# Performance work log

Measured on AMD Instinct MI355X. Metric: run time of the kernel, lower is better.

## Reference

```python
import jax, jax.numpy as jnp
from jax import lax
import numpy as np

B, T, C = 2048, 512, 32  # batch, max_seq_len, num_tags


def setup_inputs() -> dict:
    key = jax.random.key(0)
    k1, k2, k3, k4 = jax.random.split(key, 4)
    logits = jax.random.normal(k1, (B, T, C), dtype=jnp.float32)
    sequence_length = jax.random.randint(k2, (B,), 1, T + 1, dtype=jnp.int32)
    labels = jax.random.randint(k3, (B, T), 0, C, dtype=jnp.int32)
    # learned CRF transition matrix (orthogonal init approximated by normal)
    transitions = jax.random.normal(k4, (C, C), dtype=jnp.float32)
    return dict(logits=logits, sequence_length=sequence_length,
                labels=labels, transitions=transitions)


def _viterbi_decode(logits, transitions, seq_len):
    """tfa_text.crf_decode: returns highest-scoring tag sequence [B, T] int32."""
    Bn, Tn, Cn = logits.shape
    identity_bp = jnp.arange(Cn, dtype=jnp.int32)[None, :]  # carries tag through padding

    def fwd(state, xs):  # state: [B, C] viterbi scores
        logit_t, t = xs
        scores = state[:, :, None] + transitions[None]       # [B, C_prev, C_cur]
        cand = logit_t + jnp.max(scores, axis=1)             # [B, C]
        bp = jnp.argmax(scores, axis=1).astype(jnp.int32)    # [B, C] best prev tag
        active = (t < seq_len)[:, None]
        return (jnp.where(active, cand, state),
                jnp.where(active, bp, identity_bp))

    xs = (jnp.swapaxes(logits[:, 1:], 0, 1), jnp.arange(1, Tn))
    final_state, bps = lax.scan(fwd, logits[:, 0], xs)       # bps: [T-1, B, C]
    last_tag = jnp.argmax(final_state, axis=-1).astype(jnp.int32)  # [B]

    def back(tag, bp):  # tag at t+1 -> tag at t
        prev = jnp.take_along_axis(bp, tag[:, None], axis=1)[:, 0]
        return prev, tag

    first_tag, later_tags = lax.scan(back, last_tag, bps, reverse=True)
    tags = jnp.concatenate([first_tag[None], later_tags], axis=0).T  # [B, T]
    valid = jnp.arange(Tn)[None, :] < seq_len[:, None]
    return jnp.where(valid, tags, 0)


def _crf_log_likelihood(logits, labels, transitions, seq_len):
    """tfa_text.crf_log_likelihood: per-example log-likelihood [B]."""
    Bn, Tn, Cn = logits.shape

    # --- log partition via forward algorithm ---
    def fwd(alpha, xs):
        logit_t, t = xs
        new = jax.nn.logsumexp(alpha[:, :, None] + transitions[None], axis=1) + logit_t
        active = (t < seq_len)[:, None]
        return jnp.where(active, new, alpha), None

    xs = (jnp.swapaxes(logits[:, 1:], 0, 1), jnp.arange(1, Tn))
    alpha, _ = lax.scan(fwd, logits[:, 0], xs)
    log_norm = jax.nn.logsumexp(alpha, axis=-1)  # [B]

    # --- score of gold label sequence ---
    pos = jnp.arange(Tn)
    mask = (pos[None, :] < seq_len[:, None]).astype(logits.dtype)          # [B, T]
    unary = jnp.sum(
        jnp.take_along_axis(logits, labels[..., None], axis=2)[..., 0] * mask,
        axis=1)
    pair_mask = (pos[None, :-1] < (seq_len - 1)[:, None]).astype(logits.dtype)
    binary = jnp.sum(transitions[labels[:, :-1], labels[:, 1:]] * pair_mask, axis=1)

    return unary + binary - log_norm


def reference(logits, sequence_length, labels, transitions):
    # training=True path: labels clamped to >= 0 (already non-negative here)
    labels = jnp.maximum(labels, 0)
    decode_tags = _viterbi_decode(logits, transitions, sequence_length)
    log_likelihood = _crf_log_likelihood(logits, labels, transitions, sequence_length)
    loss = jnp.mean(-log_likelihood)  # recorded via add_loss in the original
    return decode_tags, loss
```

## Files before the change

kernel.cpp:

```cpp
#include <hip/hip_runtime.h>
#include <math.h>

#define BB 2048
#define TT 512
#define CC 32

#if __has_builtin(__builtin_amdgcn_exp2f)
#define EXP2F __builtin_amdgcn_exp2f
#else
#define EXP2F exp2f
#endif
#if __has_builtin(__builtin_amdgcn_logf)
#define LOG2F __builtin_amdgcn_logf
#else
#define LOG2F log2f
#endif

#define LOG2E 1.4426950408889634f
#define LN2   0.6931471805599453f

__global__ void zero_loss_kernel(float* __restrict__ out) {
  if (threadIdx.x == 0) out[(size_t)BB * TT] = 0.0f;
}

__global__ void schedule_kernel(const int* __restrict__ seqlen,
                                int* __restrict__ perm,
                                float* __restrict__ out) {
  __shared__ int s[TT];
  __shared__ int off[TT];
  const int tid = threadIdx.x;
  if (tid == 0) out[(size_t)BB * TT] = 0.0f;
  s[tid] = 0;
  __syncthreads();
  for (int b = tid; b < BB; b += TT) atomicAdd(&s[seqlen[b] - 1], 1);
  __syncthreads();
  for (int d = 1; d < TT; d <<= 1) {
    int v = s[tid] + ((tid + d < TT) ? s[tid + d] : 0);
    __syncthreads();
    s[tid] = v;
    __syncthreads();
  }
  off[tid] = (tid + 1 < TT) ? s[tid + 1] : 0;
  __syncthreads();
  for (int b = tid; b < BB; b += TT) {
    int pos = atomicAdd(&off[seqlen[b] - 1], 1);
    perm[pos] = b;
  }
}

#define ROR(dst, src, K)                                                     \
  dst = __int_as_float(__builtin_amdgcn_update_dpp(                          \
      0, __float_as_int(src), 0x120 | (K), 0xF, 0xF, false));

__global__ __launch_bounds__(128, 4) void crf_kernel(
    const float* __restrict__ logits,
    const int*   __restrict__ seqlen,
    const int*   __restrict__ labels,
    const float* __restrict__ trans,
    float*       __restrict__ out,
    const int*   __restrict__ perm)
{
  __shared__ __align__(16) unsigned char bp_s[(TT - 1) * CC];
  __shared__ __align__(16) float avs[CC];
  __shared__ unsigned char tag_s[TT];

  const int lane = threadIdx.x & 63;
  const int wv   = threadIdx.x >> 6;
  const int k    = blockIdx.x;

  const int bs0 = perm ? perm[k] : k;
  const int bs1 = perm ? perm[BB - 1 - k] : -1;

  if (wv == 0) {
    const int c = lane & 31;
    const int h = lane >> 5;

    float tr[16];
#pragma unroll
    for (int i = 0; i < 16; ++i) tr[i] = trans[(h * 16 + i) * CC + c];

    const float4* avp = (const float4*)(avs + h * 16);

    for (int sq = 0; sq < 2; ++sq) {
      const int b = sq ? bs1 : bs0;
      if (b < 0) break;
      const int len = seqlen[b];
      const float* lg = logits + (size_t)b * TT * CC;
      const size_t bT = (size_t)b * TT;

      float av = lg[c];
      if (h == 0) avs[c] = av;

      const float* lgc = lg + c;
      float l0 = 0, l1 = 0, l2 = 0;
      {
        int r1 = 1 < len ? 1 : len - 1;
        int r2 = 2 < len ? 2 : len - 1;
        int r3 = 3 < len ? 3 : len - 1;
        l0 = lgc[r1 * CC]; l1 = lgc[r2 * CC]; l2 = lgc[r3 * CC];
      }

      auto vstep = [&](int t, float logit_c) {
        float pav[16];
#pragma unroll
        for (int qq = 0; qq < 4; ++qq) ((float4*)pav)[qq] = avp[qq];

        float S[16];
#pragma unroll
        for (int i = 0; i < 16; ++i) S[i] = pav[i] + tr[i];

        float m8[8];
#pragma unroll
        for (int kk = 0; kk < 8; ++kk) m8[kk] = fmaxf(S[kk], S[kk + 8]);
#pragma unroll
        for (int kk = 0; kk < 4; ++kk) m8[kk] = fmaxf(m8[kk], m8[kk + 4]);
        float best = fmaxf(fmaxf(m8[0], m8[2]), fmaxf(m8[1], m8[3]));

        int t8[16];
#pragma unroll
        for (int i = 0; i < 16; ++i) t8[i] = (S[i] == best) ? i : 63;
#pragma unroll
        for (int kk = 0; kk < 8; ++kk) t8[kk] = min(t8[kk], t8[kk + 8]);
#pragma unroll
        for (int kk = 0; kk < 4; ++kk) t8[kk] = min(t8[kk], t8[kk + 4]);
        int bi = min(min(t8[0], t8[2]), min(t8[1], t8[3]));
        int bpi = h * 16 + bi;

        float ov = __shfl_xor(best, 32);
        int   oi = __shfl_xor(bpi, 32);
        bool take = (ov > best) || (ov == best && oi < bpi);
        best = take ? ov : best;
        bpi  = take ? oi : bpi;
        av = logit_c + best;

        if (h == 0) {
          avs[c] = av;
          bp_s[(t - 1) * CC + c] = (unsigned char)bpi;
        }
      };

      int t = 1;
      int tmain = len - 3;
      for (; t < tmain; ++t) {
        float lc = l0; l0 = l1; l1 = l2;
        l2 = lgc[(t + 3) * CC];
        vstep(t, lc);
      }
      for (; t < len; ++t) {
        float lc = l0; l0 = l1; l1 = l2;
        int rn = t + 3; rn = rn < len ? rn : len - 1;
        l2 = lgc[rn * CC];
        vstep(t, lc);
      }

      float v = av; int idx = c;
#pragma unroll
      for (int d = 1; d < 32; d <<= 1) {
        float v2 = __shfl_xor(v, d, 32);
        int   i2 = __shfl_xor(idx, d, 32);
        if (v2 > v || (v2 == v && i2 < idx)) { v = v2; idx = i2; }
      }

      if (lane == 0) {
        int tag = idx;
        tag_s[len - 1] = (unsigned char)tag;
        const uint4* bp4 = (const uint4*)bp_s;
        uint4 Ra[3], Rb[3];
#pragma unroll
        for (int kk = 0; kk < 3; ++kk) {
          int r = len - 2 - kk;
          if (r >= 0) { Ra[kk] = bp4[2 * r]; Rb[kk] = bp4[2 * r + 1]; }
        }
        for (int tt = len - 1; tt > 0; --tt) {
          uint4 ua = Ra[0], ub = Rb[0];
          Ra[0] = Ra[1]; Rb[0] = Rb[1];
          Ra[1] = Ra[2]; Rb[1] = Rb[2];
          int r = tt - 4;
          if (r >= 0) { Ra[2] = bp4[2 * r]; Rb[2] = bp4[2 * r + 1]; }
          uint4 u4;
          u4.x = (tag & 16) ? ub.x : ua.x;
          u4.y = (tag & 16) ? ub.y : ua.y;
          u4.z = (tag & 16) ? ub.z : ua.z;
          u4.w = (tag & 16) ? ub.w : ua.w;
          unsigned lo = (tag & 8) ? u4.z : u4.x;
          unsigned hi = (tag & 8) ? u4.w : u4.y;
          unsigned u1 = (tag & 4) ? hi : lo;
          tag = (int)((u1 >> ((tag & 3) * 8)) & 0xffu);
          tag_s[tt - 1] = (unsigned char)tag;
        }
      }

#pragma unroll
      for (int j = 0; j < 8; ++j) {
        int tt = lane + 64 * j;
        float val = (tt < len) ? (float)tag_s[tt] : 0.0f;
        out[bT + tt] = val;
      }
    }

  } else {
    const int i = lane & 15;
    const int r = (lane >> 4) & 1;
    const int c = lane & 31;
    const int pr = (lane < 32) ? r : (1 - r);
    const int bpaddr = ((lane < 32) ? lane : (lane ^ 16)) << 2;

    float E[16];
#pragma unroll
    for (int kk = 0; kk < 16; ++kk) {
      int p = pr * 16 + ((i - kk) & 15);
      E[kk] = EXP2F(trans[p * CC + c] * LOG2E);
    }

    float loss_acc = 0.0f;

    for (int sq = 0; sq < 2; ++sq) {
      const int b = sq ? bs1 : bs0;
      if (b < 0) break;
      const int len = seqlen[b];
      const float* lg = logits + (size_t)b * TT * CC;
      const int* lab = labels + (size_t)b * TT;

      float P   = EXP2F(lg[c] * LOG2E);
      float Acc = 0.0f;

      const float* lgc = lg + c;
      float e0 = 0, e1 = 0, e2 = 0;
      {
        int r1 = 1 < len ? 1 : len - 1;
        int r2 = 2 < len ? 2 : len - 1;
        int r3 = 3 < len ? 3 : len - 1;
        e0 = EXP2F(lgc[r1 * CC] * LOG2E);
        e1 = EXP2F(lgc[r2 * CC] * LOG2E);
        e2 = EXP2F(lgc[r3 * CC] * LOG2E);
      }

      auto fstep = [&](float el) {
        float base = __int_as_float(
            __builtin_amdgcn_ds_bpermute(bpaddr, __float_as_int(P)));
        float x;
        float a0 = base * E[0];
        ROR(x, base, 1);  float a1 = x * E[1];
        ROR(x, base, 2);  float a2 = x * E[2];
        ROR(x, base, 3);  float a3 = x * E[3];
        ROR(x, base, 4);  a0 = fmaf(x, E[4],  a0);
        ROR(x, base, 5);  a1 = fmaf(x, E[5],  a1);
        ROR(x, base, 6);  a2 = fmaf(x, E[6],  a2);
        ROR(x, base, 7);  a3 = fmaf(x, E[7],  a3);
        ROR(x, base, 8);  a0 = fmaf(x, E[8],  a0);
        ROR(x, base, 9);  a1 = fmaf(x, E[9],  a1);
        ROR(x, base, 10); a2 = fmaf(x, E[10], a2);
        ROR(x, base, 11); a3 = fmaf(x, E[11], a3);
        ROR(x, base, 12); a0 = fmaf(x, E[12], a0);
        ROR(x, base, 13); a1 = fmaf(x, E[13], a1);
        ROR(x, base, 14); a2 = fmaf(x, E[14], a2);
        ROR(x, base, 15); a3 = fmaf(x, E[15], a3);
        float part = (a0 + a1) + (a2 + a3);
        float oth  = __shfl_xor(part, 32);
        float s    = part + oth;
        P = el * s;
      };

      auto renorm = [&]() {
        float m = P;
#pragma unroll
        for (int d = 1; d < 32; d <<= 1) m = fmaxf(m, __shfl_xor(m, d, 32));
        int e = (int)(__float_as_uint(m) >> 23) - 127;
        P = ldexpf(P, -e);
        Acc += (float)e;
      };

      int t = 1;
      int tmain = len - 3;
      for (; t < tmain; ++t) {
        float ec = e0; e0 = e1; e1 = e2;
        e2 = EXP2F(lgc[(t + 3) * CC] * LOG2E);
        fstep(ec);
        if ((t & 3) == 0) renorm();
      }
      for (; t < len; ++t) {
        float ec = e0; e0 = e1; e1 = e2;
        int rn = t + 3; rn = rn < len ? rn : len - 1;
        e2 = EXP2F(lgc[rn * CC] * LOG2E);
        fstep(ec);
        if ((t & 3) == 0) renorm();
      }

      float uacc = 0.0f, bacc = 0.0f;
#pragma unroll
      for (int j = 0; j < 8; ++j) {
        int tt = lane + 64 * j;
        if (tt < len) {
          int lt = lab[tt];
          uacc += lg[tt * CC + lt];
          if (tt + 1 < len) {
            int ln = lab[tt + 1];
            bacc += trans[lt * CC + ln];
          }
        }
      }
#pragma unroll
      for (int d = 32; d >= 1; d >>= 1) {
        uacc += __shfl_xor(uacc, d);
        bacc += __shfl_xor(bacc, d);
      }

      float ss = P;
#pragma unroll
      for (int d = 1; d < 32; d <<= 1) ss += __shfl_xor(ss, d, 32);
      float log_norm = LN2 * (Acc + LOG2F(ss));

      loss_acc += (uacc + bacc - log_norm);
    }

    if (lane == 0) {
      atomicAdd(out + (size_t)BB * TT, loss_acc * (-1.0f / BB));
    }
  }
}

extern "C" void kernel_launch(void* const* d_in, const int* in_sizes, int n_in,
                              void* d_out, int out_size, void* d_ws, size_t ws_size,
                              hipStream_t stream) {
  const float* logits = (const float*)d_in[0];
  const int*   seqlen = (const int*)d_in[1];
  const int*   labels = (const int*)d_in[2];
  const float* trans  = (const float*)d_in[3];
  float* out = (float*)d_out;

  if (d_ws != nullptr && ws_size >= BB * sizeof(int)) {
    int* perm = (int*)d_ws;
    schedule_kernel<<<1, TT, 0, stream>>>(seqlen, perm, out);
    crf_kernel<<<dim3(BB / 2), dim3(128), 0, stream>>>(
        logits, seqlen, labels, trans, out, perm);
  } else {
    zero_loss_kernel<<<1, 64, 0, stream>>>(out);
    crf_kernel<<<dim3(BB), dim3(128), 0, stream>>>(
        logits, seqlen, labels, trans, out, nullptr);
  }
}
```

Before: 421.4 us.

## Replace LDS exchanges with DPP rotates and permlane swaps in CRF recurrences

The Viterbi wave no longer round-trips the previous scores through shared memory each step. Each lane now gets them with a 16-lane DPP rotate pattern plus a permlane16 swap, with backpointer indices taken from a precomputed permutation. The forward (logsumexp) wave swaps its ds_bpermute and xor-32 shuffles for permlane16/32 swap instructions, and the renorm and final reductions use DPP rotate trees. The goal is to cut LDS latency on the serial per-timestep dependency chain, at the cost of relying on gfx950-specific builtins with slower fallbacks.

```diff
diff --git a/kernel.cpp b/kernel.cpp
--- a/kernel.cpp
+++ b/kernel.cpp
@@ -52,6 +52,35 @@
   dst = __int_as_float(__builtin_amdgcn_update_dpp(                          \
       0, __float_as_int(src), 0x120 | (K), 0xF, 0xF, false));
 
+__device__ __forceinline__ float xor16f(float x, int lane) {
+#if __has_builtin(__builtin_amdgcn_permlane16_swap)
+  auto r = __builtin_amdgcn_permlane16_swap(__float_as_uint(x),
+                                            __float_as_uint(x), false, false);
+  return __uint_as_float((lane & 16) ? r[0] : r[1]);
+#else
+  return __int_as_float(
+      __builtin_amdgcn_ds_swizzle(__float_as_int(x), 0x401F));
+#endif
+}
+__device__ __forceinline__ float xor32f(float x, int lane) {
+#if __has_builtin(__builtin_amdgcn_permlane32_swap)
+  auto r = __builtin_amdgcn_permlane32_swap(__float_as_uint(x),
+                                            __float_as_uint(x), false, false);
+  return __uint_as_float((lane & 32) ? r[0] : r[1]);
+#else
+  return __shfl_xor(x, 32);
+#endif
+}
+__device__ __forceinline__ int xor32i(int x, int lane) {
+#if __has_builtin(__builtin_amdgcn_permlane32_swap)
+  auto r = __builtin_amdgcn_permlane32_swap((unsigned)x, (unsigned)x,
+                                            false, false);
+  return (int)((lane & 32) ? r[0] : r[1]);
+#else
+  return __shfl_xor(x, 32);
+#endif
+}
+
 __global__ __launch_bounds__(128, 4) void crf_kernel(
     const float* __restrict__ logits,
     const int*   __restrict__ seqlen,
@@ -61,7 +90,6 @@
     const int*   __restrict__ perm)
 {
   __shared__ __align__(16) unsigned char bp_s[(TT - 1) * CC];
-  __shared__ __align__(16) float avs[CC];
   __shared__ unsigned char tag_s[TT];
 
   const int lane = threadIdx.x & 63;
@@ -71,15 +99,20 @@
   const int bs0 = perm ? perm[k] : k;
   const int bs1 = perm ? perm[BB - 1 - k] : -1;
 
+  const int i  = lane & 15;
+  const int c  = lane & 31;
+  const int r  = (lane >> 4) & 1;
+  const int pr = (lane < 32) ? r : 1 - r;
+
   if (wv == 0) {
-    const int c = lane & 31;
-    const int h = lane >> 5;
-
-    float tr[16];
-#pragma unroll
-    for (int i = 0; i < 16; ++i) tr[i] = trans[(h * 16 + i) * CC + c];
-
-    const float4* avp = (const float4*)(avs + h * 16);
+    float tr2[16];
+    int   pidx[16];
+#pragma unroll
+    for (int kk = 0; kk < 16; ++kk) {
+      int p = pr * 16 + ((i - kk) & 15);
+      pidx[kk] = p;
+      tr2[kk] = trans[p * CC + c];
+    }
 
     for (int sq = 0; sq < 2; ++sq) {
       const int b = sq ? bs1 : bs0;
@@ -89,7 +122,6 @@
       const size_t bT = (size_t)b * TT;
 
       float av = lg[c];
-      if (h == 0) avs[c] = av;
 
       const float* lgc = lg + c;
       float l0 = 0, l1 = 0, l2 = 0;
@@ -101,13 +133,25 @@
       }
 
       auto vstep = [&](int t, float logit_c) {
-        float pav[16];
-#pragma unroll
-        for (int qq = 0; qq < 4; ++qq) ((float4*)pav)[qq] = avp[qq];
-
+        float base = (lane < 32) ? av : xor16f(av, lane);
         float S[16];
-#pragma unroll
-        for (int i = 0; i < 16; ++i) S[i] = pav[i] + tr[i];
+        float x;
+        S[0] = base + tr2[0];
+        ROR(x, base, 1);  S[1]  = x + tr2[1];
+        ROR(x, base, 2);  S[2]  = x + tr2[2];
+        ROR(x, base, 3);  S[3]  = x + tr2[3];
+        ROR(x, base, 4);  S[4]  = x + tr2[4];
+        ROR(x, base, 5);  S[5]  = x + tr2[5];
+        ROR(x, base, 6);  S[6]  = x + tr2[6];
+        ROR(x, base, 7);  S[7]  = x + tr2[7];
+        ROR(x, base, 8);  S[8]  = x + tr2[8];
+        ROR(x, base, 9);  S[9]  = x + tr2[9];
+        ROR(x, base, 10); S[10] = x + tr2[10];
+        ROR(x, base, 11); S[11] = x + tr2[11];
+        ROR(x, base, 12); S[12] = x + tr2[12];
+        ROR(x, base, 13); S[13] = x + tr2[13];
+        ROR(x, base, 14); S[14] = x + tr2[14];
+        ROR(x, base, 15); S[15] = x + tr2[15];
 
         float m8[8];
 #pragma unroll
@@ -118,25 +162,22 @@
 
         int t8[16];
 #pragma unroll
-        for (int i = 0; i < 16; ++i) t8[i] = (S[i] == best) ? i : 63;
+        for (int kk = 0; kk < 16; ++kk)
+          t8[kk] = (S[kk] == best) ? pidx[kk] : 63;
 #pragma unroll
         for (int kk = 0; kk < 8; ++kk) t8[kk] = min(t8[kk], t8[kk + 8]);
 #pragma unroll
         for (int kk = 0; kk < 4; ++kk) t8[kk] = min(t8[kk], t8[kk + 4]);
         int bi = min(min(t8[0], t8[2]), min(t8[1], t8[3]));
-        int bpi = h * 16 + bi;
-
-        float ov = __shfl_xor(best, 32);
-        int   oi = __shfl_xor(bpi, 32);
-        bool take = (ov > best) || (ov == best && oi < bpi);
+
+        float ov = xor32f(best, lane);
+        int   oi = xor32i(bi, lane);
+        bool take = (ov > best) || (ov == best && oi < bi);
         best = take ? ov : best;
-        bpi  = take ? oi : bpi;
+        int bpi = take ? oi : bi;
         av = logit_c + best;
 
-        if (h == 0) {
-          avs[c] = av;
-          bp_s[(t - 1) * CC + c] = (unsigned char)bpi;
-        }
+        if (lane < 32) bp_s[(t - 1) * CC + c] = (unsigned char)bpi;
       };
 
       int t = 1;
@@ -168,15 +209,15 @@
         uint4 Ra[3], Rb[3];
 #pragma unroll
         for (int kk = 0; kk < 3; ++kk) {
-          int r = len - 2 - kk;
-          if (r >= 0) { Ra[kk] = bp4[2 * r]; Rb[kk] = bp4[2 * r + 1]; }
+          int rr = len - 2 - kk;
+          if (rr >= 0) { Ra[kk] = bp4[2 * rr]; Rb[kk] = bp4[2 * rr + 1]; }
         }
         for (int tt = len - 1; tt > 0; --tt) {
           uint4 ua = Ra[0], ub = Rb[0];
           Ra[0] = Ra[1]; Rb[0] = Rb[1];
           Ra[1] = Ra[2]; Rb[1] = Rb[2];
-          int r = tt - 4;
-          if (r >= 0) { Ra[2] = bp4[2 * r]; Rb[2] = bp4[2 * r + 1]; }
+          int rr = tt - 4;
+          if (rr >= 0) { Ra[2] = bp4[2 * rr]; Rb[2] = bp4[2 * rr + 1]; }
           uint4 u4;
           u4.x = (tag & 16) ? ub.x : ua.x;
           u4.y = (tag & 16) ? ub.y : ua.y;
@@ -199,12 +240,6 @@
     }
 
   } else {
-    const int i = lane & 15;
-    const int r = (lane >> 4) & 1;
-    const int c = lane & 31;
-    const int pr = (lane < 32) ? r : (1 - r);
-    const int bpaddr = ((lane < 32) ? lane : (lane ^ 16)) << 2;
-
     float E[16];
 #pragma unroll
     for (int kk = 0; kk < 16; ++kk) {
@@ -236,8 +271,7 @@
       }
 
       auto fstep = [&](float el) {
-        float base = __int_as_float(
-            __builtin_amdgcn_ds_bpermute(bpaddr, __float_as_int(P)));
+        float base = (lane < 32) ? P : xor16f(P, lane);
         float x;
         float a0 = base * E[0];
         ROR(x, base, 1);  float a1 = x * E[1];
@@ -256,15 +290,17 @@
         ROR(x, base, 14); a2 = fmaf(x, E[14], a2);
         ROR(x, base, 15); a3 = fmaf(x, E[15], a3);
         float part = (a0 + a1) + (a2 + a3);
-        float oth  = __shfl_xor(part, 32);
-        float s    = part + oth;
-        P = el * s;
+        float oth  = xor32f(part, lane);
+        P = el * (part + oth);
       };
 
       auto renorm = [&]() {
-        float m = P;
-#pragma unroll
-        for (int d = 1; d < 32; d <<= 1) m = fmaxf(m, __shfl_xor(m, d, 32));
+        float m = P, y;
+        ROR(y, m, 8); m = fmaxf(m, y);
+        ROR(y, m, 4); m = fmaxf(m, y);
+        ROR(y, m, 2); m = fmaxf(m, y);
+        ROR(y, m, 1); m = fmaxf(m, y);
+        m = fmaxf(m, xor16f(m, lane));
         int e = (int)(__float_as_uint(m) >> 23) - 127;
         P = ldexpf(P, -e);
         Acc += (float)e;
@@ -305,9 +341,12 @@
         bacc += __shfl_xor(bacc, d);
       }
 
-      float ss = P;
-#pragma unroll
-      for (int d = 1; d < 32; d <<= 1) ss += __shfl_xor(ss, d, 32);
+      float ss = P, y2;
+      ROR(y2, ss, 8); ss += y2;
+      ROR(y2, ss, 4); ss += y2;
+      ROR(y2, ss, 2); ss += y2;
+      ROR(y2, ss, 1); ss += y2;
+      ss += xor16f(ss, lane);
       float log_norm = LN2 * (Acc + LOG2F(ss));
 
       loss_acc += (uacc + bacc - log_norm);
```

After: 429.7 us. About the same (+1.9%).
